# Kernel optimization log

Measured on AMD Instinct MI355X. Metric: run time of the kernel, lower is better.

The kernel has to match this reference:

```python
import jax, jax.numpy as jnp
import numpy as np

N = 50000          # residues
E = 1000000        # edges
H = 128            # hidden_channels
CUT = 11.5         # cutoff
NR = 6             # num_radial
NS = 3             # num_spherical
NPE = 16           # num_pos_emb

def swish(x):
    return x * jax.nn.sigmoid(x)

def rbf(d):
    # Bessel-style radial basis with smooth cosine cutoff, [E, NR]
    u = jnp.clip(d / CUT, 0.0, 1.0)
    n = jnp.arange(1, NR + 1, dtype=jnp.float32)
    fc = 0.5 * (jnp.cos(jnp.pi * u) + 1.0)
    return jnp.sqrt(2.0 / CUT) * jnp.sin(n * jnp.pi * u[:, None]) / (d[:, None] + 1e-6) * fc[:, None]

def angle_emb(d, ang):
    # d_angle_emb: radial x cos(l*angle) -> [E, NR*NS]
    r = rbf(d)
    l = jnp.arange(NS, dtype=jnp.float32)
    a = jnp.cos(ang[:, None] * l)
    return (r[:, :, None] * a[:, None, :]).reshape(d.shape[0], NR * NS)

def theta_phi_emb(d, theta, phi):
    # d_theta_phi_emb: radial x angular(theta) x angular(phi) -> [E, NR*NS*NS]
    r = rbf(d)
    l = jnp.arange(NS, dtype=jnp.float32)
    ct = jnp.cos(theta[:, None] * l)
    cp = jnp.cos(phi[:, None] * l)
    return jnp.einsum('en,el,em->enlm', r, ct, cp).reshape(d.shape[0], NR * NS * NS)


def setup_inputs():
    key = jax.random.key(0)
    ks = jax.random.split(key, 20)
    f32 = jnp.float32
    pos = jax.random.normal(ks[0], (N, 3), f32) * 8.0
    pos_n = pos + jax.random.normal(ks[1], (N, 3), f32) * 0.8
    pos_c = pos + jax.random.normal(ks[2], (N, 3), f32) * 0.8
    z = jax.random.randint(ks[3], (N,), 0, 26)
    bb_embs = jax.random.normal(ks[4], (N, 6), f32)
    side_chain_embs = jax.random.normal(ks[5], (N, 8), f32)
    esm_embs = jax.random.normal(ks[6], (N, 1280), f32)
    batch = jnp.zeros((N,), jnp.int32)
    edge_index = jax.random.randint(ks[7], (2, E), 0, N)
    def w(k, shape):
        return jax.random.normal(k, shape, f32) * (1.0 / np.sqrt(shape[0]))
    edge_in = NR * NS * NS + 3 * NR * NS + NPE  # 54 + 54 + 16 = 124
    params = dict(
        W_emb=w(ks[8], (26 + 6 + 8, H // 2)), b_emb=jnp.zeros((H // 2,), f32),
        W_esm=w(ks[9], (1280, H // 2)), b_esm=jnp.zeros((H // 2,), f32),
        W_edge=w(ks[10], (edge_in, H)),
        W_msg=w(ks[11], (H, H)),
        W_upd=w(ks[12], (H, H)),
        W_o0=w(ks[13], (H, H)), b_o0=jnp.zeros((H,), f32),
        W_o1=w(ks[14], (H, 32)), b_o1=jnp.zeros((32,), f32),
        W_of=w(ks[15], (32, 1)), b_of=jnp.zeros((1,), f32),
        W_n0=w(ks[16], (H, 32)), b_n0=jnp.zeros((32,), f32),
        W_nf=w(ks[17], (32, 2)), b_nf=jnp.zeros((2,), f32),
    )
    return dict(z=z, pos=pos, pos_n=pos_n, pos_c=pos_c, bb_embs=bb_embs,
                side_chain_embs=side_chain_embs, esm_embs=esm_embs,
                batch=batch, edge_index=edge_index, **params)


def reference(z, pos, pos_n, pos_c, bb_embs, side_chain_embs, esm_embs, batch,
              edge_index, W_emb, b_emb, W_esm, b_esm, W_edge, W_msg, W_upd,
              W_o0, b_o0, W_o1, b_o1, W_of, b_of, W_n0, b_n0, W_nf, b_nf):
    # --- node embedding fusion (level='allatom+esm') ---
    oh = jax.nn.one_hot(z, 26, dtype=jnp.float32)
    x_a = jnp.concatenate([oh, bb_embs, side_chain_embs], axis=1) @ W_emb + b_emb
    x_s = esm_embs @ W_esm + b_esm
    x = jnp.concatenate([x_a, x_s], axis=-1)  # [N, H]

    j, i = edge_index[0], edge_index[1]

    # --- sinusoidal positional embedding of sequence offsets ---
    dpe = (j - i).astype(jnp.float32)
    freq = jnp.exp(jnp.arange(0, NPE, 2, dtype=jnp.float32) * (-np.log(10000.0) / NPE))
    ang = dpe[:, None] * freq
    pe = jnp.concatenate([jnp.cos(ang), jnp.sin(ang)], axis=-1)  # [E, NPE]

    # --- distance / theta / phi (triplet gathers via sequence neighbors) ---
    v_ji = pos[j] - pos[i]
    dist = jnp.linalg.norm(pos[i] - pos[j], axis=1)
    refi0 = (i - 1) % N
    refi1 = (i + 1) % N
    v_r0 = pos[refi0] - pos[i]
    v_r1 = pos[refi1] - pos[i]
    a = jnp.sum(v_ji * v_r0, axis=-1)
    b = jnp.linalg.norm(jnp.cross(v_ji, v_r0), axis=-1)
    theta = jnp.arctan2(b, a)
    p1 = jnp.cross(v_r0, v_r1)
    p2 = jnp.cross(v_r0, v_ji)
    a = jnp.sum(p1 * p2, axis=-1)
    b = jnp.sum(jnp.cross(p1, p2) * v_r0, axis=-1) / (jnp.linalg.norm(v_r0, axis=-1) + 1e-7)
    phi = jnp.arctan2(b, a)
    feature0 = theta_phi_emb(dist, theta, phi)  # [E, 54]

    # --- backbone-frame Euler angles (allatom branch) ---
    o1x = pos_n[i] - pos[i]
    o1z = jnp.cross(o1x, jnp.cross(o1x, pos_c[i] - pos[i]))
    o1zl = jnp.linalg.norm(o1z, axis=1) + 1e-7
    o2x = pos_n[j] - pos[j]
    o2z = jnp.cross(o2x, jnp.cross(o2x, pos_c[j] - pos[j]))
    o2zl = jnp.linalg.norm(o2z, axis=1) + 1e-7
    nvec = jnp.cross(o1z, o2z)
    angle1 = jnp.arctan2(jnp.sum(jnp.cross(o1x, nvec) * o1z, -1) / o1zl, jnp.sum(o1x * nvec, -1))
    angle2 = jnp.arctan2(jnp.linalg.norm(nvec, axis=-1), jnp.sum(o1z * o2z, -1))
    angle3 = jnp.arctan2(jnp.sum(jnp.cross(nvec, o2x) * o2z, -1) / o2zl, jnp.sum(nvec * o2x, -1))
    feature1 = jnp.concatenate([angle_emb(dist, angle1), angle_emb(dist, angle2),
                                angle_emb(dist, angle3)], axis=1)  # [E, 54]

    # --- message passing (gather-compute-scatter stand-in for model_E) ---
    ef = swish(jnp.concatenate([feature0, feature1, pe], axis=-1) @ W_edge)  # [E, H]
    m = swish(x[j] @ W_msg) * ef
    agg = jax.ops.segment_sum(m, i, num_segments=N)
    xe = x + swish(agg @ W_upd)

    # --- output heads (dropout inactive at inference) ---
    xn = jax.nn.relu(x @ W_n0 + b_n0)
    node_out = xn @ W_nf + b_nf                   # [N, 2]
    h = jax.nn.relu(xe @ W_o0 + b_o0)
    h = jax.nn.relu(h @ W_o1 + b_o1)
    out = jax.nn.sigmoid(h @ W_of + b_of)         # [N, 1]
    return out, node_out
```

## Files before the change

### kernel.cpp

```cpp
#include <hip/hip_runtime.h>
#include <math.h>
#include <stdint.h>

#define NRES 50000
#define NEDGE 1000000
#define PI_F 3.14159265358979323846f
#define NSEG 196

typedef __attribute__((ext_vector_type(8))) short short8;
typedef __attribute__((ext_vector_type(4))) float floatx4;
typedef __attribute__((ext_vector_type(2))) short bf16x2;
typedef __attribute__((address_space(1))) bf16x2* gbf16x2p;

struct f3 { float x, y, z; };
__device__ __forceinline__ f3 ld3(const float* __restrict__ p, int i) {
  return {p[3*i+0], p[3*i+1], p[3*i+2]};
}
__device__ __forceinline__ f3 f3sub(f3 a, f3 b){ return {a.x-b.x, a.y-b.y, a.z-b.z}; }
__device__ __forceinline__ f3 f3cross(f3 a, f3 b){
  return {a.y*b.z - a.z*b.y, a.z*b.x - a.x*b.z, a.x*b.y - a.y*b.x};
}
__device__ __forceinline__ float f3dot(f3 a, f3 b){ return a.x*b.x + a.y*b.y + a.z*b.z; }
__device__ __forceinline__ float swish_fast(float v){
  return v * __builtin_amdgcn_rcpf(1.0f + __expf(-v));
}
__device__ __forceinline__ short f2bf(float f){
  unsigned u = __float_as_uint(f);
  unsigned r = (u + 0x7fffu + ((u >> 16) & 1u)) >> 16;
  return (short)r;
}
__device__ __forceinline__ float bf2f(short s){
  return __uint_as_float(((unsigned)(unsigned short)s) << 16);
}
__device__ __forceinline__ float cos_atan2(float y, float x){
  return x * __builtin_amdgcn_rsqf(fmaxf(x*x + y*y, 1e-30f));
}
__device__ __forceinline__ void atom_pk_bf16(short* addr, bf16x2 v){
  __builtin_amdgcn_global_atomic_fadd_v2bf16((gbf16x2p)(uintptr_t)addr, v);
}
__device__ __forceinline__ unsigned pkbf(float lo, float hi){
  unsigned r;
  asm("v_cvt_pk_bf16_f32 %0, %1, %2" : "=v"(r) : "v"(lo), "v"(hi));
  return r;
}

__device__ __forceinline__ void edge_features(
    int e, int j, int i,
    const float* __restrict__ pos, const float* __restrict__ posn,
    const float* __restrict__ posc, short (*sF)[136])
{
  f3 pj = ld3(pos, j), pi = ld3(pos, i);
  f3 vji = f3sub(pj, pi);
  float nji2 = f3dot(vji, vji);
  float dist = sqrtf(nji2);
  int r0i = (i == 0) ? (NRES - 1) : (i - 1);
  int r1i = (i == NRES - 1) ? 0 : (i + 1);
  f3 vr0 = f3sub(ld3(pos, r0i), pi);
  f3 vr1 = f3sub(ld3(pos, r1i), pi);
  float nr02 = f3dot(vr0, vr0);

  float ct = f3dot(vji, vr0) * __builtin_amdgcn_rsqf(fmaxf(nji2 * nr02, 1e-30f));
  f3 p1 = f3cross(vr0, vr1);
  f3 p2 = f3cross(vr0, vji);
  float pa = f3dot(p1, p2);
  float pb = f3dot(f3cross(p1, p2), vr0) / (sqrtf(nr02) + 1e-7f);
  float cp = cos_atan2(pb, pa);

  f3 pni = ld3(posn, i), pci = ld3(posc, i);
  f3 o1x = f3sub(pni, pi);
  f3 o1z = f3cross(o1x, f3cross(o1x, f3sub(pci, pi)));
  float no1z2 = f3dot(o1z, o1z);
  float o1zl = sqrtf(no1z2) + 1e-7f;
  f3 pnj = ld3(posn, j), pcj = ld3(posc, j);
  f3 o2x = f3sub(pnj, pj);
  f3 o2z = f3cross(o2x, f3cross(o2x, f3sub(pcj, pj)));
  float no2z2 = f3dot(o2z, o2z);
  float o2zl = sqrtf(no2z2) + 1e-7f;
  f3 nv = f3cross(o1z, o2z);
  float y1 = f3dot(f3cross(o1x, nv), o1z) / o1zl;
  float ca1 = cos_atan2(y1, f3dot(o1x, nv));
  float ca2 = f3dot(o1z, o2z) * __builtin_amdgcn_rsqf(fmaxf(no1z2 * no2z2, 1e-30f));
  float y3 = f3dot(f3cross(nv, o2x), o2z) / o2zl;
  float ca3 = cos_atan2(y3, f3dot(nv, o2x));

  float u = fminf(dist * (1.0f/11.5f), 1.0f);
  float spu, cpu;
  __sincosf(PI_F * u, &spu, &cpu);
  float fc = 0.5f * (cpu + 1.0f);
  float pref = 0.41702882811414954f * __builtin_amdgcn_rcpf(dist + 1e-6f) * fc;
  float rb[6];
  {
    float twoc = 2.0f * cpu;
    float s_nm1 = 0.0f, s_n = spu;
    #pragma unroll
    for (int nn = 0; nn < 6; ++nn) {
      rb[nn] = pref * s_n;
      float s_np1 = twoc * s_n - s_nm1;
      s_nm1 = s_n; s_n = s_np1;
    }
  }

  float pend = 0.0f;
  float ctv[3] = {1.0f, ct, 2.0f*ct*ct - 1.0f};
  float cpv[3] = {1.0f, cp, 2.0f*cp*cp - 1.0f};
  #pragma unroll
  for (int nn = 0; nn < 6; ++nn)
    #pragma unroll
    for (int l = 0; l < 3; ++l)
      #pragma unroll
      for (int m = 0; m < 3; ++m) {
        const int f = nn*9 + l*3 + m;
        float v = rb[nn] * ctv[l] * cpv[m];
        if (f & 1) *(unsigned*)&sF[e][f-1] = pkbf(pend, v);
        else       pend = v;
      }

  float cas[3] = {ca1, ca2, ca3};
  #pragma unroll
  for (int t = 0; t < 3; ++t) {
    float c = cas[t];
    float cav[3] = {1.0f, c, 2.0f*c*c - 1.0f};
    #pragma unroll
    for (int nn = 0; nn < 6; ++nn)
      #pragma unroll
      for (int l = 0; l < 3; ++l) {
        const int f = 54 + t*18 + nn*3 + l;
        float v = rb[nn] * cav[l];
        if (f & 1) *(unsigned*)&sF[e][f-1] = pkbf(pend, v);
        else       pend = v;
      }
  }

  const float FRQ[8] = {1.0f, 0.31622776601683794f, 0.1f, 0.03162277660168379f,
                        0.01f, 0.003162277660168379f, 0.001f, 0.0003162277660168379f};
  float dpe = (float)(j - i);
  float cb[8], sb[8];
  #pragma unroll
  for (int q = 0; q < 8; ++q) __sincosf(dpe * FRQ[q], &sb[q], &cb[q]);
  #pragma unroll
  for (int q = 0; q < 8; q += 2) {
    *(unsigned*)&sF[e][108 + q] = pkbf(cb[q], cb[q+1]);
    *(unsigned*)&sF[e][116 + q] = pkbf(sb[q], sb[q+1]);
  }
  *(unsigned*)&sF[e][124] = 0u;
  *(unsigned*)&sF[e][126] = 0u;
}

__global__ __launch_bounds__(256) void k_wprep(
    const float* __restrict__ We, const float* __restrict__ Wm,
    const float* __restrict__ Ws, const float* __restrict__ Wu,
    const float* __restrict__ Wo0, const float* __restrict__ Wn0,
    const float* __restrict__ Wo1,
    short* __restrict__ Wef, short* __restrict__ Wmf, short* __restrict__ Wsf,
    short* __restrict__ Wuf, short* __restrict__ Wo0f,
    short* __restrict__ Wn0f, short* __restrict__ Wo1f)
{
  int gid = blockIdx.x * 256 + threadIdx.x;
  const float* src; short* dst; int NT, K, N, t;
  if      (gid < 16384)  { t = gid;          src = We;  dst = Wef;  NT = 8; K = 124;  N = 128; }
  else if (gid < 32768)  { t = gid - 16384;  src = Wm;  dst = Wmf;  NT = 8; K = 128;  N = 128; }
  else if (gid < 114688) { t = gid - 32768;  src = Ws;  dst = Wsf;  NT = 4; K = 1280; N = 64;  }
  else if (gid < 131072) { t = gid - 114688; src = Wu;  dst = Wuf;  NT = 8; K = 128;  N = 128; }
  else if (gid < 147456) { t = gid - 131072; src = Wo0; dst = Wo0f; NT = 8; K = 128;  N = 128; }
  else if (gid < 151552) { t = gid - 147456; src = Wn0; dst = Wn0f; NT = 2; K = 128;  N = 32;  }
  else if (gid < 155648) { t = gid - 151552; src = Wo1; dst = Wo1f; NT = 2; K = 128;  N = 32;  }
  else return;
  int j = t & 7, lane = (t >> 3) & 63;
  int rest = t >> 9;
  int nt = rest % NT, kt = rest / NT;
  int k = kt*32 + (lane >> 4)*8 + j, n = nt*16 + (lane & 15);
  dst[t] = f2bf((k < K) ? src[k*N + n] : 0.0f);
}

__global__ __launch_bounds__(256) void k_hist(
    const int* __restrict__ ei, int* __restrict__ bins)
{
  int e = blockIdx.x * 256 + threadIdx.x;
  if (e < NEDGE) atomicAdd(&bins[ei[NEDGE + e]], 1);
}

__global__ __launch_bounds__(256) void k_scan1(
    int* __restrict__ bins, int* __restrict__ bsum)
{
  __shared__ int s[256];
  const int t = threadIdx.x, b = blockIdx.x;
  const int idx = b * 256 + t;
  int v = (idx < NRES) ? bins[idx] : 0;
  s[t] = v;
  __syncthreads();
  #pragma unroll
  for (int d = 1; d < 256; d <<= 1) {
    int add = (t >= d) ? s[t - d] : 0;
    __syncthreads();
    if (t >= d) s[t] += add;
    __syncthreads();
  }
  if (idx < NRES) bins[idx] = s[t] - v;
  if (t == 255) bsum[b] = s[255];
}

__global__ __launch_bounds__(256) void k_scan2(int* __restrict__ bsum)
{
  __shared__ int s[256];
  const int t = threadIdx.x;
  int v = (t < NSEG) ? bsum[t] : 0;
  s[t] = v;
  __syncthreads();
  #pragma unroll
  for (int d = 1; d < 256; d <<= 1) {
    int add = (t >= d) ? s[t - d] : 0;
    __syncthreads();
    if (t >= d) s[t] += add;
    __syncthreads();
  }
  if (t < NSEG) bsum[t] = s[t] - v;
}

__global__ __launch_bounds__(256) void k_scan3(
    int* __restrict__ bins, const int* __restrict__ bsum)
{
  int idx = blockIdx.x * 256 + threadIdx.x;
  if (idx < NRES) bins[idx] += bsum[blockIdx.x];
}

__global__ __launch_bounds__(256) void k_scatter(
    const int* __restrict__ ei, int* __restrict__ bins, int2* __restrict__ sij)
{
  int e = blockIdx.x * 256 + threadIdx.x;
  if (e < NEDGE) {
    int j = ei[e], i = ei[NEDGE + e];
    int slot = atomicAdd(&bins[i], 1);
    if (slot >= 0 && slot < NEDGE) sij[slot] = make_int2(j, i);
  }
}

__global__ __launch_bounds__(256) void k_xa(
    const int* __restrict__ z, const float* __restrict__ bb,
    const float* __restrict__ side, const float* __restrict__ W_emb,
    const float* __restrict__ b_emb, short* __restrict__ xb)
{
  int tid = threadIdx.x;
  int h = tid & 63;
  int n = blockIdx.x * 4 + (tid >> 6);
  if (n >= NRES) return;
  int zz = z[n];
  float acc = W_emb[zz * 64 + h] + b_emb[h];
  #pragma unroll
  for (int k = 0; k < 6; ++k) acc += bb[n*6 + k] * W_emb[(26 + k)*64 + h];
  #pragma unroll
  for (int k = 0; k < 8; ++k) acc += side[n*8 + k] * W_emb[(32 + k)*64 + h];
  xb[(size_t)n * 128 + h] = f2bf(acc);
}

__global__ __launch_bounds__(256) void k_esm(
    const float* __restrict__ esm, const short* __restrict__ Wsf,
    const float* __restrict__ b, short* __restrict__ xb)
{
  const int tid = threadIdx.x;
  const int lane = tid & 63, w = tid >> 6;
  const int quad = lane >> 4, colb = lane & 15;
  const int tile0 = blockIdx.x * 64 + w * 16;

  int arow = tile0 + colb;
  if (arow >= NRES) arow = NRES - 1;
  const float* ap = esm + (size_t)arow * 1280 + quad * 8;

  floatx4 acc[4];
  #pragma unroll
  for (int nt = 0; nt < 4; ++nt) acc[nt] = (floatx4){0.f, 0.f, 0.f, 0.f};

  for (int kt = 0; kt < 40; ++kt) {
    float4 v0 = *(const float4*)(ap + kt*32);
    float4 v1 = *(const float4*)(ap + kt*32 + 4);
    short8 a;
    a[0] = f2bf(v0.x); a[1] = f2bf(v0.y); a[2] = f2bf(v0.z); a[3] = f2bf(v0.w);
    a[4] = f2bf(v1.x); a[5] = f2bf(v1.y); a[6] = f2bf(v1.z); a[7] = f2bf(v1.w);
    #pragma unroll
    for (int nt = 0; nt < 4; ++nt) {
      short8 bf = *(const short8*)&Wsf[(size_t)((kt*4 + nt)*64 + lane)*8];
      acc[nt] = __builtin_amdgcn_mfma_f32_16x16x32_bf16(a, bf, acc[nt], 0, 0, 0);
    }
  }
  #pragma unroll
  for (int nt = 0; nt < 4; ++nt) {
    int ch = nt*16 + colb;
    float bias = b[ch];
    #pragma unroll
    for (int r = 0; r < 4; ++r) {
      int n = tile0 + quad*4 + r;
      if (n < NRES) xb[(size_t)n * 128 + 64 + ch] = f2bf(acc[nt][r] + bias);
    }
  }
}

__global__ __launch_bounds__(256) void k_node(
    const float* __restrict__ esm, const short* __restrict__ Wsf,
    const float* __restrict__ b_esm,
    const int* __restrict__ z, const float* __restrict__ bb,
    const float* __restrict__ side, const float* __restrict__ W_emb,
    const float* __restrict__ b_emb,
    const short* __restrict__ Wmf,
    short* __restrict__ xb, short* __restrict__ xmb)
{
  __shared__ __align__(16) short sX[64][136];

  const int tid = threadIdx.x;
  const int lane = tid & 63, w = tid >> 6;
  const int quad = lane >> 4, colb = lane & 15;
  const int n0 = blockIdx.x * 64;
  const int tile0 = n0 + w * 16;

  int arow = tile0 + colb;
  if (arow >= NRES) arow = NRES - 1;
  const float* ap = esm + (size_t)arow * 1280 + quad * 8;

  floatx4 acc[4];
  #pragma unroll
  for (int nt = 0; nt < 4; ++nt) acc[nt] = (floatx4){0.f, 0.f, 0.f, 0.f};

  for (int kt = 0; kt < 40; ++kt) {
    float4 v0 = *(const float4*)(ap + kt*32);
    float4 v1 = *(const float4*)(ap + kt*32 + 4);
    short8 a;
    a[0] = f2bf(v0.x); a[1] = f2bf(v0.y); a[2] = f2bf(v0.z); a[3] = f2bf(v0.w);
    a[4] = f2bf(v1.x); a[5] = f2bf(v1.y); a[6] = f2bf(v1.z); a[7] = f2bf(v1.w);
    #pragma unroll
    for (int nt = 0; nt < 4; ++nt) {
      short8 bf = *(const short8*)&Wsf[(size_t)((kt*4 + nt)*64 + lane)*8];
      acc[nt] = __builtin_amdgcn_mfma_f32_16x16x32_bf16(a, bf, acc[nt], 0, 0, 0);
    }
  }

  #pragma unroll
  for (int nt = 0; nt < 4; ++nt) {
    int ch = nt*16 + colb;
    float bias = b_esm[ch];
    #pragma unroll
    for (int r = 0; r < 4; ++r)
      sX[w*16 + quad*4 + r][64 + ch] = f2bf(acc[nt][r] + bias);
  }
  {
    int r2 = tid >> 2;
    int n2 = n0 + r2; if (n2 >= NRES) n2 = NRES - 1;
    int c0 = (tid & 3) * 16;
    int zz = z[n2];
    float bbv[6], sdv[8];
    #pragma unroll
    for (int k = 0; k < 6; ++k) bbv[k] = bb[n2*6 + k];
    #pragma unroll
    for (int k = 0; k < 8; ++k) sdv[k] = side[n2*8 + k];
    #pragma unroll
    for (int c = 0; c < 16; c += 2) {
      float v0, v1;
      #pragma unroll
      for (int h = 0; h < 2; ++h) {
        int col = c0 + c + h;
        float a2 = W_emb[zz*64 + col] + b_emb[col];
        #pragma unroll
        for (int k = 0; k < 6; ++k) a2 += bbv[k] * W_emb[(26 + k)*64 + col];
        #pragma unroll
        for (int k = 0; k < 8; ++k) a2 += sdv[k] * W_emb[(32 + k)*64 + col];
        if (h) v1 = a2; else v0 = a2;
      }
      *(unsigned*)&sX[r2][c0 + c] = pkbf(v0, v1);
    }
  }
  __syncthreads();

  #pragma unroll
  for (int it = 0; it < 4; ++it) {
    int idx = it * 256 + tid;
    int row = idx >> 4, c8 = idx & 15;
    int n = n0 + row;
    if (n < NRES) *(short8*)&xb[(size_t)n * 128 + c8*8] = *(const short8*)&sX[row][c8*8];
  }

  floatx4 accM[4][2];
  #pragma unroll
  for (int mt = 0; mt < 4; ++mt) {
    accM[mt][0] = (floatx4){0.f,0.f,0.f,0.f};
    accM[mt][1] = (floatx4){0.f,0.f,0.f,0.f};
  }
  #pragma unroll
  for (int kt = 0; kt < 4; ++kt) {
    short8 b0 = *(const short8*)&Wmf[(size_t)((kt*8 + w*2 + 0)*64 + lane)*8];
    short8 b1 = *(const short8*)&Wmf[(size_t)((kt*8 + w*2 + 1)*64 + lane)*8];
    #pragma unroll
    for (int mt = 0; mt < 4; ++mt) {
      short8 a = *(const short8*)&sX[mt*16 + colb][kt*32 + quad*8];
      accM[mt][0] = __builtin_amdgcn_mfma_f32_16x16x32_bf16(a, b0, accM[mt][0], 0, 0, 0);
      accM[mt][1] = __builtin_amdgcn_mfma_f32_16x16x32_bf16(a, b1, accM[mt][1], 0, 0, 0);
    }
  }
  __syncthreads();

  #pragma unroll
  for (int mt = 0; mt < 4; ++mt)
    #pragma unroll
    for (int nt = 0; nt < 2; ++nt)
      #pragma unroll
      for (int r = 0; r < 4; ++r)
        sX[mt*16 + quad*4 + r][w*32 + nt*16 + colb] = f2bf(swish_fast(accM[mt][nt][r]));
  __syncthreads();
  #pragma unroll
  for (int it = 0; it < 4; ++it) {
    int idx = it * 256 + tid;
    int row = idx >> 4, c8 = idx & 15;
    int n = n0 + row;
    if (n < NRES) *(short8*)&xmb[(size_t)n * 128 + c8*8] = *(const short8*)&sX[row][c8*8];
  }
}

__global__ __launch_bounds__(256, 4) void k_edge_s(
    const int2* __restrict__ sij,
    const float* __restrict__ pos,
    const float* __restrict__ posn, const float* __restrict__ posc,
    const short* __restrict__ xmb, const short* __restrict__ Wef,
    short* __restrict__ aggb)
{
  __shared__ int sJ[64];
  __shared__ int sI[64];
  __shared__ __align__(16) short sF[64][136];
  __shared__ __align__(16) short sXJ[64][136];

  const int tid = threadIdx.x;
  const int orig = blockIdx.x;
  const int xcd = orig & 7, sub = orig >> 3;
  const int wg = (xcd == 0 ? 0 : 1954 + (xcd - 1) * 1953) + sub;
  const int e0 = wg * 64;

  if (tid < 64) {
    int2 ji = sij[e0 + tid];
    int jj = ji.x, ii = ji.y;
    sJ[tid] = (jj < 0) ? 0 : ((jj >= NRES) ? NRES - 1 : jj);
    sI[tid] = (ii < 0) ? 0 : ((ii >= NRES) ? NRES - 1 : ii);
  }
  __syncthreads();

  if (tid < 64) {
    edge_features(tid, sJ[tid], sI[tid], pos, posn, posc, sF);
  } else {
    const int t2 = tid - 64;
    for (int it = 0; it < 6; ++it) {
      int idx = it * 192 + t2;
      if (idx < 1024) {
        int row = idx >> 4;
        int c8 = idx & 15;
        *(short8*)&sXJ[row][c8*8] = *(const short8*)&xmb[(size_t)sJ[row] * 128 + c8*8];
      }
    }
  }
  __syncthreads();

  const int lane = tid & 63, w = tid >> 6;
  const int quad = lane >> 4, colb = lane & 15;
  const int nb = w * 2;

  short8 bE[4][2];
  #pragma unroll
  for (int kt = 0; kt < 4; ++kt)
    #pragma unroll
    for (int nt = 0; nt < 2; ++nt)
      bE[kt][nt] = *(const short8*)&Wef[(size_t)((kt*8 + nb + nt)*64 + lane)*8];

  floatx4 accE[4][2];
  #pragma unroll
  for (int mt = 0; mt < 4; ++mt) {
    accE[mt][0] = (floatx4){0.f, 0.f, 0.f, 0.f};
    accE[mt][1] = (floatx4){0.f, 0.f, 0.f, 0.f};
  }

  #pragma unroll
  for (int kt = 0; kt < 4; ++kt) {
    #pragma unroll
    for (int mt = 0; mt < 4; ++mt) {
      short8 af = *(const short8*)&sF[mt*16 + colb][kt*32 + quad*8];
      #pragma unroll
      for (int nt = 0; nt < 2; ++nt)
        accE[mt][nt] = __builtin_amdgcn_mfma_f32_16x16x32_bf16(af, bE[kt][nt], accE[mt][nt], 0, 0, 0);
    }
  }
  __syncthreads();

  short (*sM)[136] = sF;
  #pragma unroll
  for (int mt = 0; mt < 4; ++mt)
    #pragma unroll
    for (int nt = 0; nt < 2; ++nt) {
      int ch = w*32 + nt*16 + colb;
      #pragma unroll
      for (int r = 0; r < 4; ++r) {
        int e = mt*16 + quad*4 + r;
        float mv = bf2f(sXJ[e][ch]) * swish_fast(accE[mt][nt][r]);
        sM[e][ch] = f2bf(mv);
      }
    }
  __syncthreads();

  {
    const int p = tid & 63;
    const int g = tid >> 6;
    float ax = 0.f, ay = 0.f;
    int cur = sI[g * 16];
    #pragma unroll
    for (int rr = 0; rr < 16; ++rr) {
      int row = g * 16 + rr;
      int ii = sI[row];
      if (ii != cur) {
        bf16x2 v; v[0] = f2bf(ax); v[1] = f2bf(ay);
        atom_pk_bf16(&aggb[(size_t)cur * 128 + p*2], v);
        ax = 0.f; ay = 0.f; cur = ii;
      }
      bf16x2 mv = *(const bf16x2*)&sM[row][p*2];
      ax += bf2f(mv[0]); ay += bf2f(mv[1]);
    }
    bf16x2 v; v[0] = f2bf(ax); v[1] = f2bf(ay);
    atom_pk_bf16(&aggb[(size_t)cur * 128 + p*2], v);
  }
}

__global__ __launch_bounds__(256, 4) void k_edge_b(
    const int* __restrict__ ei, const float* __restrict__ pos,
    const float* __restrict__ posn, const float* __restrict__ posc,
    const short* __restrict__ xb, const short* __restrict__ Wef,
    const short* __restrict__ Wmf, short* __restrict__ aggb)
{
  __shared__ int sJ[64];
  __shared__ int sI[64];
  __shared__ __align__(16) short sF[64][136];
  __shared__ __align__(16) short sXJ[64][136];

  const int tid = threadIdx.x;
  const int e0 = blockIdx.x * 64;

  if (tid < 64) { sJ[tid] = ei[e0 + tid]; sI[tid] = ei[NEDGE + e0 + tid]; }
  __syncthreads();

  if (tid < 64) {
    edge_features(tid, sJ[tid], sI[tid], pos, posn, posc, sF);
  } else {
    const int t2 = tid - 64;
    for (int it = 0; it < 6; ++it) {
      int idx = it * 192 + t2;
      if (idx < 1024) {
        int row = idx >> 4;
        int c8 = idx & 15;
        *(short8*)&sXJ[row][c8*8] = *(const short8*)&xb[(size_t)sJ[row] * 128 + c8*8];
      }
    }
  }
  __syncthreads();

  const int lane = tid & 63, w = tid >> 6;
  const int quad = lane >> 4, colb = lane & 15;
  const int nb = w * 2;

  short8 bE[4][2], bM[4][2];
  #pragma unroll
  for (int kt = 0; kt < 4; ++kt)
    #pragma unroll
    for (int nt = 0; nt < 2; ++nt) {
      bE[kt][nt] = *(const short8*)&Wef[(size_t)((kt*8 + nb + nt)*64 + lane)*8];
      bM[kt][nt] = *(const short8*)&Wmf[(size_t)((kt*8 + nb + nt)*64 + lane)*8];
    }

  floatx4 accE[4][2], accM[4][2];
  #pragma unroll
  for (int mt = 0; mt < 4; ++mt)
    #pragma unroll
    for (int nt = 0; nt < 2; ++nt) {
      accE[mt][nt] = (floatx4){0.f, 0.f, 0.f, 0.f};
      accM[mt][nt] = (floatx4){0.f, 0.f, 0.f, 0.f};
    }

  #pragma unroll
  for (int kt = 0; kt < 4; ++kt) {
    #pragma unroll
    for (int mt = 0; mt < 4; ++mt) {
      short8 af = *(const short8*)&sF [mt*16 + colb][kt*32 + quad*8];
      short8 ax = *(const short8*)&sXJ[mt*16 + colb][kt*32 + quad*8];
      #pragma unroll
      for (int nt = 0; nt < 2; ++nt) {
        accE[mt][nt] = __builtin_amdgcn_mfma_f32_16x16x32_bf16(af, bE[kt][nt], accE[mt][nt], 0, 0, 0);
        accM[mt][nt] = __builtin_amdgcn_mfma_f32_16x16x32_bf16(ax, bM[kt][nt], accM[mt][nt], 0, 0, 0);
      }
    }
  }
  __syncthreads();

  short (*sM)[136] = sXJ;
  #pragma unroll
  for (int mt = 0; mt < 4; ++mt)
    #pragma unroll
    for (int nt = 0; nt < 2; ++nt) {
      int ch = w*32 + nt*16 + colb;
      #pragma unroll
      for (int r = 0; r < 4; ++r) {
        int e = mt*16 + quad*4 + r;
        sM[e][ch] = f2bf(swish_fast(accM[mt][nt][r]) * swish_fast(accE[mt][nt][r]));
      }
    }
  __syncthreads();

  #pragma unroll
  for (int it = 0; it < 16; ++it) {
    int flat = it * 256 + tid;
    int row = flat >> 6, p = flat & 63;
    bf16x2 v = *(const bf16x2*)&sM[row][p*2];
    atom_pk_bf16(&aggb[(size_t)sI[row] * 128 + p*2], v);
  }
}

__global__ __launch_bounds__(256) void k_upd(
    const short* __restrict__ xb, const short* __restrict__ aggb,
    const short* __restrict__ Wuf, const short* __restrict__ Wo0f,
    const short* __restrict__ Wn0f, const short* __restrict__ Wo1f,
    const float* __restrict__ bn0, const float* __restrict__ Wnf,
    const float* __restrict__ bnf, const float* __restrict__ bo0,
    const float* __restrict__ bo1, const float* __restrict__ Wof,
    const float* __restrict__ bof, float* __restrict__ out0,
    float* __restrict__ out1)
{
  __shared__ __align__(16) short sA[64][136];
  __shared__ __align__(16) short sX[64][136];
  __shared__ float sS[64][33];

  const int tid = threadIdx.x;
  const int lane = tid & 63, w = tid >> 6;
  const int quad = lane >> 4, colb = lane & 15;
  const int n0 = blockIdx.x * 64;

  #pragma unroll
  for (int it = 0; it < 4; ++it) {
    int idx = it * 256 + tid;
    int row = idx >> 4, c8 = idx & 15;
    int n = n0 + row;
    short8 va = (short8)(short)0, vx = (short8)(short)0;
    if (n < NRES) {
      va = *(const short8*)&aggb[(size_t)n * 128 + c8*8];
      vx = *(const short8*)&xb  [(size_t)n * 128 + c8*8];
    }
    *(short8*)&sA[row][c8*8] = va;
    *(short8*)&sX[row][c8*8] = vx;
  }
  __syncthreads();

  {
    floatx4 accN[2];
    accN[0] = (floatx4){0.f,0.f,0.f,0.f}; accN[1] = (floatx4){0.f,0.f,0.f,0.f};
    #pragma unroll
    for (int kt = 0; kt < 4; ++kt) {
      short8 a = *(const short8*)&sX[w*16 + colb][kt*32 + quad*8];
      #pragma unroll
      for (int nt = 0; nt < 2; ++nt) {
        short8 bf = *(const short8*)&Wn0f[(size_t)((kt*2 + nt)*64 + lane)*8];
        accN[nt] = __builtin_amdgcn_mfma_f32_16x16x32_bf16(a, bf, accN[nt], 0, 0, 0);
      }
    }
    #pragma unroll
    for (int nt = 0; nt < 2; ++nt) {
      int col = nt*16 + colb;
      float bias = bn0[col];
      #pragma unroll
      for (int r = 0; r < 4; ++r)
        sS[w*16 + quad*4 + r][col] = fmaxf(accN[nt][r] + bias, 0.0f);
    }
  }
  __syncthreads();
  if (tid < 128) {
    int row = tid >> 1, oc = tid & 1;
    int n = n0 + row;
    if (n < NRES) {
      float a2 = bnf[oc];
      #pragma unroll
      for (int k = 0; k < 32; ++k) a2 += sS[row][k] * Wnf[k*2 + oc];
      out1[(size_t)n * 2 + oc] = a2;
    }
  }

  floatx4 acc1[4][2];
  #pragma unroll
  for (int mt = 0; mt < 4; ++mt) {
    acc1[mt][0] = (floatx4){0.f,0.f,0.f,0.f};
    acc1[mt][1] = (floatx4){0.f,0.f,0.f,0.f};
  }
  #pragma unroll
  for (int kt = 0; kt < 4; ++kt) {
    short8 b0 = *(const short8*)&Wuf[(size_t)((kt*8 + w*2 + 0)*64 + lane)*8];
    short8 b1 = *(const short8*)&Wuf[(size_t)((kt*8 + w*2 + 1)*64 + lane)*8];
    #pragma unroll
    for (int mt = 0; mt < 4; ++mt) {
      short8 a = *(const short8*)&sA[mt*16 + colb][kt*32 + quad*8];
      acc1[mt][0] = __builtin_amdgcn_mfma_f32_16x16x32_bf16(a, b0, acc1[mt][0], 0, 0, 0);
      acc1[mt][1] = __builtin_amdgcn_mfma_f32_16x16x32_bf16(a, b1, acc1[mt][1], 0, 0, 0);
    }
  }
  __syncthreads();
  #pragma unroll
  for (int mt = 0; mt < 4; ++mt)
    #pragma unroll
    for (int nt = 0; nt < 2; ++nt)
      #pragma unroll
      for (int r = 0; r < 4; ++r) {
        int row = mt*16 + quad*4 + r, col = w*32 + nt*16 + colb;
        float xv = bf2f(sX[row][col]);
        sA[row][col] = f2bf(xv + swish_fast(acc1[mt][nt][r]));
      }
  __syncthreads();

  floatx4 acc2[4][2];
  #pragma unroll
  for (int mt = 0; mt < 4; ++mt) {
    acc2[mt][0] = (floatx4){0.f,0.f,0.f,0.f};
    acc2[mt][1] = (floatx4){0.f,0.f,0.f,0.f};
  }
  #pragma unroll
  for (int kt = 0; kt < 4; ++kt) {
    short8 b0 = *(const short8*)&Wo0f[(size_t)((kt*8 + w*2 + 0)*64 + lane)*8];
    short8 b1 = *(const short8*)&Wo0f[(size_t)((kt*8 + w*2 + 1)*64 + lane)*8];
    #pragma unroll
    for (int mt = 0; mt < 4; ++mt) {
      short8 a = *(const short8*)&sA[mt*16 + colb][kt*32 + quad*8];
      acc2[mt][0] = __builtin_amdgcn_mfma_f32_16x16x32_bf16(a, b0, acc2[mt][0], 0, 0, 0);
      acc2[mt][1] = __builtin_amdgcn_mfma_f32_16x16x32_bf16(a, b1, acc2[mt][1], 0, 0, 0);
    }
  }
  __syncthreads();
  #pragma unroll
  for (int mt = 0; mt < 4; ++mt)
    #pragma unroll
    for (int nt = 0; nt < 2; ++nt) {
      int col = w*32 + nt*16 + colb;
      float bias = bo0[col];
      #pragma unroll
      for (int r = 0; r < 4; ++r) {
        int row = mt*16 + quad*4 + r;
        sX[row][col] = f2bf(fmaxf(acc2[mt][nt][r] + bias, 0.0f));
      }
    }
  __syncthreads();

  {
    floatx4 accH[2];
    accH[0] = (floatx4){0.f,0.f,0.f,0.f}; accH[1] = (floatx4){0.f,0.f,0.f,0.f};
    #pragma unroll
    for (int kt = 0; kt < 4; ++kt) {
      short8 a = *(const short8*)&sX[w*16 + colb][kt*32 + quad*8];
      #pragma unroll
      for (int nt = 0; nt < 2; ++nt) {
        short8 bf = *(const short8*)&Wo1f[(size_t)((kt*2 + nt)*64 + lane)*8];
        accH[nt] = __builtin_amdgcn_mfma_f32_16x16x32_bf16(a, bf, accH[nt], 0, 0, 0);
      }
    }
    __syncthreads();
    #pragma unroll
    for (int nt = 0; nt < 2; ++nt) {
      int col = nt*16 + colb;
      float bias = bo1[col];
      #pragma unroll
      for (int r = 0; r < 4; ++r)
        sS[w*16 + quad*4 + r][col] = fmaxf(accH[nt][r] + bias, 0.0f);
    }
  }
  __syncthreads();

  if (tid < 64) {
    int n = n0 + tid;
    if (n < NRES) {
      float a2 = bof[0];
      #pragma unroll
      for (int k = 0; k < 32; ++k) a2 += sS[tid][k] * Wof[k];
      out0[n] = 1.0f / (1.0f + expf(-a2));
    }
  }
}

extern "C" void kernel_launch(void* const* d_in, const int* in_sizes, int n_in,
                              void* d_out, int out_size, void* d_ws, size_t ws_size,
                              hipStream_t stream) {
  (void)in_sizes; (void)n_in; (void)out_size;
  const int*   z     = (const int*)  d_in[0];
  const float* pos   = (const float*)d_in[1];
  const float* posn  = (const float*)d_in[2];
  const float* posc  = (const float*)d_in[3];
  const float* bb    = (const float*)d_in[4];
  const float* side  = (const float*)d_in[5];
  const float* esm   = (const float*)d_in[6];
  const int*   ei    = (const int*)  d_in[8];
  const float* W_emb = (const float*)d_in[9];
  const float* b_emb = (const float*)d_in[10];
  const float* W_esm = (const float*)d_in[11];
  const float* b_esm = (const float*)d_in[12];
  const float* W_edge= (const float*)d_in[13];
  const float* W_msg = (const float*)d_in[14];
  const float* W_upd = (const float*)d_in[15];
  const float* W_o0  = (const float*)d_in[16];
  const float* b_o0  = (const float*)d_in[17];
  const float* W_o1  = (const float*)d_in[18];
  const float* b_o1  = (const float*)d_in[19];
  const float* W_of  = (const float*)d_in[20];
  const float* b_of  = (const float*)d_in[21];
  const float* W_n0  = (const float*)d_in[22];
  const float* b_n0  = (const float*)d_in[23];
  const float* W_nf  = (const float*)d_in[24];
  const float* b_nf  = (const float*)d_in[25];

  float* out0 = (float*)d_out;
  float* out1 = out0 + NRES;
  char* ws = (char*)d_ws;

  const bool full = (ws_size >= (size_t)46912096);

  if (full) {
    short* xb   = (short*)ws;
    short* aggb = (short*)(ws + 12800000);
    short* xmb  = (short*)(ws + 25600000);
    short* Wef  = (short*)(ws + 38400000);
    short* Wmf  = (short*)(ws + 38432768);
    short* Wsf  = (short*)(ws + 38465536);
    short* Wuf  = (short*)(ws + 38629376);
    short* Wo0f = (short*)(ws + 38662144);
    short* Wn0f = (short*)(ws + 38694912);
    short* Wo1f = (short*)(ws + 38703104);
    int*   bins = (int*)  (ws + 38711296);
    int*   bsum = (int*)  (ws + 38911296);
    int2*  sij  = (int2*) (ws + 38912096);

    hipMemsetAsync(aggb, 0, (size_t)NRES * 128 * sizeof(short), stream);
    hipMemsetAsync(bins, 0, (size_t)NRES * sizeof(int), stream);

    k_wprep  <<<608, 256, 0, stream>>>(W_edge, W_msg, W_esm, W_upd, W_o0, W_n0, W_o1,
                                       Wef, Wmf, Wsf, Wuf, Wo0f, Wn0f, Wo1f);
    k_hist   <<<3907, 256, 0, stream>>>(ei, bins);
    k_scan1  <<<NSEG, 256, 0, stream>>>(bins, bsum);
    k_scan2  <<<1,    256, 0, stream>>>(bsum);
    k_scan3  <<<NSEG, 256, 0, stream>>>(bins, bsum);
    k_scatter<<<3907, 256, 0, stream>>>(ei, bins, sij);
    k_node   <<<782,  256, 0, stream>>>(esm, Wsf, b_esm, z, bb, side, W_emb, b_emb,
                                        Wmf, xb, xmb);
    k_edge_s <<<15625, 256, 0, stream>>>(sij, pos, posn, posc, xmb, Wef, aggb);
    k_upd    <<<782,   256, 0, stream>>>(xb, aggb, Wuf, Wo0f, Wn0f, Wo1f,
                                         b_n0, W_nf, b_nf, b_o0, b_o1, W_of, b_of,
                                         out0, out1);
  } else {
    short* xb   = (short*)ws;
    short* aggb = (short*)(ws + 12800000);
    short* Wef  = (short*)(ws + 25600000);
    short* Wmf  = (short*)(ws + 25632768);
    short* Wsf  = (short*)(ws + 25665536);
    short* Wuf  = (short*)(ws + 25829376);
    short* Wo0f = (short*)(ws + 25862144);
    short* Wn0f = (short*)(ws + 25894912);
    short* Wo1f = (short*)(ws + 25903104);

    hipMemsetAsync(aggb, 0, (size_t)NRES * 128 * sizeof(short), stream);

    k_wprep <<<608, 256, 0, stream>>>(W_edge, W_msg, W_esm, W_upd, W_o0, W_n0, W_o1,
                                      Wef, Wmf, Wsf, Wuf, Wo0f, Wn0f, Wo1f);
    k_xa    <<<12500, 256, 0, stream>>>(z, bb, side, W_emb, b_emb, xb);
    k_esm   <<<782,   256, 0, stream>>>(esm, Wsf, b_esm, xb);
    k_edge_b<<<15625, 256, 0, stream>>>(ei, pos, posn, posc, xb, Wef, Wmf, aggb);
    k_upd   <<<782,   256, 0, stream>>>(xb, aggb, Wuf, Wo0f, Wn0f, Wo1f,
                                        b_n0, W_nf, b_nf, b_o0, b_o1, W_of, b_of,
                                        out0, out1);
  }
}
```

Measured before the change: 706.6 us.

## Split k_node ESM GEMM reduction across two wave groups with 512 threads

k_node now runs 512 threads per block, so each 16-row tile is computed by two waves that each take half of the 1280-wide ESM reduction. The two partial sums are combined through a new shared-memory buffer. The loop also prefetches the next float4 pair of ESM inputs in registers, and the embedding and W_msg work is spread over 8 waves. The aim is more memory-level parallelism and shorter per-wave serial chains in this bandwidth-bound node kernel, at the cost of extra shared memory and a synchronization.

Measured after the change: 706.7 us. Within noise of the previous version (+0.0%).

```diff
diff --git a/kernel.cpp b/kernel.cpp
--- a/kernel.cpp
+++ b/kernel.cpp
@@ -293,7 +293,7 @@
   }
 }
 
-__global__ __launch_bounds__(256) void k_node(
+__global__ __launch_bounds__(512) void k_node(
     const float* __restrict__ esm, const short* __restrict__ Wsf,
     const float* __restrict__ b_esm,
     const int* __restrict__ z, const float* __restrict__ bb,
@@ -303,46 +303,67 @@
     short* __restrict__ xb, short* __restrict__ xmb)
 {
   __shared__ __align__(16) short sX[64][136];
+  __shared__ float sP[4][16][68];
 
   const int tid = threadIdx.x;
   const int lane = tid & 63, w = tid >> 6;
   const int quad = lane >> 4, colb = lane & 15;
+  const int t = w & 3, kh = w >> 2;
   const int n0 = blockIdx.x * 64;
-  const int tile0 = n0 + w * 16;
+  const int tile0 = n0 + t * 16;
 
   int arow = tile0 + colb;
   if (arow >= NRES) arow = NRES - 1;
-  const float* ap = esm + (size_t)arow * 1280 + quad * 8;
+  const float* ap = esm + (size_t)arow * 1280 + kh * 640 + quad * 8;
 
   floatx4 acc[4];
   #pragma unroll
   for (int nt = 0; nt < 4; ++nt) acc[nt] = (floatx4){0.f, 0.f, 0.f, 0.f};
 
-  for (int kt = 0; kt < 40; ++kt) {
-    float4 v0 = *(const float4*)(ap + kt*32);
-    float4 v1 = *(const float4*)(ap + kt*32 + 4);
+  float4 v0 = *(const float4*)(ap);
+  float4 v1 = *(const float4*)(ap + 4);
+  for (int kt = 0; kt < 20; ++kt) {
+    float4 nv0 = v0, nv1 = v1;
+    if (kt < 19) {
+      nv0 = *(const float4*)(ap + (kt+1)*32);
+      nv1 = *(const float4*)(ap + (kt+1)*32 + 4);
+    }
     short8 a;
     a[0] = f2bf(v0.x); a[1] = f2bf(v0.y); a[2] = f2bf(v0.z); a[3] = f2bf(v0.w);
     a[4] = f2bf(v1.x); a[5] = f2bf(v1.y); a[6] = f2bf(v1.z); a[7] = f2bf(v1.w);
+    const int kc = kh*20 + kt;
     #pragma unroll
     for (int nt = 0; nt < 4; ++nt) {
-      short8 bf = *(const short8*)&Wsf[(size_t)((kt*4 + nt)*64 + lane)*8];
+      short8 bf = *(const short8*)&Wsf[(size_t)((kc*4 + nt)*64 + lane)*8];
       acc[nt] = __builtin_amdgcn_mfma_f32_16x16x32_bf16(a, bf, acc[nt], 0, 0, 0);
     }
-  }
-
-  #pragma unroll
-  for (int nt = 0; nt < 4; ++nt) {
-    int ch = nt*16 + colb;
-    float bias = b_esm[ch];
-    #pragma unroll
-    for (int r = 0; r < 4; ++r)
-      sX[w*16 + quad*4 + r][64 + ch] = f2bf(acc[nt][r] + bias);
+    v0 = nv0; v1 = nv1;
+  }
+
+  if (kh == 1) {
+    #pragma unroll
+    for (int nt = 0; nt < 4; ++nt)
+      #pragma unroll
+      for (int r = 0; r < 4; ++r)
+        sP[t][quad*4 + r][nt*16 + colb] = acc[nt][r];
+  }
+  __syncthreads();
+
+  if (kh == 0) {
+    #pragma unroll
+    for (int nt = 0; nt < 4; ++nt) {
+      int ch = nt*16 + colb;
+      float bias = b_esm[ch];
+      #pragma unroll
+      for (int r = 0; r < 4; ++r)
+        sX[t*16 + quad*4 + r][64 + ch] =
+            f2bf(acc[nt][r] + sP[t][quad*4 + r][ch] + bias);
+    }
   }
   {
-    int r2 = tid >> 2;
+    int r2 = tid >> 3;
     int n2 = n0 + r2; if (n2 >= NRES) n2 = NRES - 1;
-    int c0 = (tid & 3) * 16;
+    int c0 = (tid & 7) * 8;
     int zz = z[n2];
     float bbv[6], sdv[8];
     #pragma unroll
@@ -350,8 +371,8 @@
     #pragma unroll
     for (int k = 0; k < 8; ++k) sdv[k] = side[n2*8 + k];
     #pragma unroll
-    for (int c = 0; c < 16; c += 2) {
-      float v0, v1;
+    for (int c = 0; c < 8; c += 2) {
+      float u0, u1;
       #pragma unroll
       for (int h = 0; h < 2; ++h) {
         int col = c0 + c + h;
@@ -360,36 +381,31 @@
         for (int k = 0; k < 6; ++k) a2 += bbv[k] * W_emb[(26 + k)*64 + col];
         #pragma unroll
         for (int k = 0; k < 8; ++k) a2 += sdv[k] * W_emb[(32 + k)*64 + col];
-        if (h) v1 = a2; else v0 = a2;
-      }
-      *(unsigned*)&sX[r2][c0 + c] = pkbf(v0, v1);
-    }
-  }
-  __syncthreads();
-
-  #pragma unroll
-  for (int it = 0; it < 4; ++it) {
-    int idx = it * 256 + tid;
+        if (h) u1 = a2; else u0 = a2;
+      }
+      *(unsigned*)&sX[r2][c0 + c] = pkbf(u0, u1);
+    }
+  }
+  __syncthreads();
+
+  #pragma unroll
+  for (int it = 0; it < 2; ++it) {
+    int idx = it * 512 + tid;
     int row = idx >> 4, c8 = idx & 15;
     int n = n0 + row;
     if (n < NRES) *(short8*)&xb[(size_t)n * 128 + c8*8] = *(const short8*)&sX[row][c8*8];
   }
 
-  floatx4 accM[4][2];
-  #pragma unroll
-  for (int mt = 0; mt < 4; ++mt) {
-    accM[mt][0] = (floatx4){0.f,0.f,0.f,0.f};
-    accM[mt][1] = (floatx4){0.f,0.f,0.f,0.f};
-  }
+  floatx4 accM[4];
+  #pragma unroll
+  for (int mt = 0; mt < 4; ++mt) accM[mt] = (floatx4){0.f,0.f,0.f,0.f};
   #pragma unroll
   for (int kt = 0; kt < 4; ++kt) {
-    short8 b0 = *(const short8*)&Wmf[(size_t)((kt*8 + w*2 + 0)*64 + lane)*8];
-    short8 b1 = *(const short8*)&Wmf[(size_t)((kt*8 + w*2 + 1)*64 + lane)*8];
+    short8 b0 = *(const short8*)&Wmf[(size_t)((kt*8 + w)*64 + lane)*8];
     #pragma unroll
     for (int mt = 0; mt < 4; ++mt) {
       short8 a = *(const short8*)&sX[mt*16 + colb][kt*32 + quad*8];
-      accM[mt][0] = __builtin_amdgcn_mfma_f32_16x16x32_bf16(a, b0, accM[mt][0], 0, 0, 0);
-      accM[mt][1] = __builtin_amdgcn_mfma_f32_16x16x32_bf16(a, b1, accM[mt][1], 0, 0, 0);
+      accM[mt] = __builtin_amdgcn_mfma_f32_16x16x32_bf16(a, b0, accM[mt], 0, 0, 0);
     }
   }
   __syncthreads();
@@ -397,14 +413,12 @@
   #pragma unroll
   for (int mt = 0; mt < 4; ++mt)
     #pragma unroll
-    for (int nt = 0; nt < 2; ++nt)
-      #pragma unroll
-      for (int r = 0; r < 4; ++r)
-        sX[mt*16 + quad*4 + r][w*32 + nt*16 + colb] = f2bf(swish_fast(accM[mt][nt][r]));
-  __syncthreads();
-  #pragma unroll
-  for (int it = 0; it < 4; ++it) {
-    int idx = it * 256 + tid;
+    for (int r = 0; r < 4; ++r)
+      sX[mt*16 + quad*4 + r][w*16 + colb] = f2bf(swish_fast(accM[mt][r]));
+  __syncthreads();
+  #pragma unroll
+  for (int it = 0; it < 2; ++it) {
+    int idx = it * 512 + tid;
     int row = idx >> 4, c8 = idx & 15;
     int n = n0 + row;
     if (n < NRES) *(short8*)&xmb[(size_t)n * 128 + c8*8] = *(const short8*)&sX[row][c8*8];
@@ -836,7 +850,7 @@
     k_scan2  <<<1,    256, 0, stream>>>(bsum);
     k_scan3  <<<NSEG, 256, 0, stream>>>(bins, bsum);
     k_scatter<<<3907, 256, 0, stream>>>(ei, bins, sij);
-    k_node   <<<782,  256, 0, stream>>>(esm, Wsf, b_esm, z, bb, side, W_emb, b_emb,
+    k_node   <<<782,  512, 0, stream>>>(esm, Wsf, b_esm, z, bb, side, W_emb, b_emb,
                                         Wmf, xb, xmb);
     k_edge_s <<<15625, 256, 0, stream>>>(sij, pos, posn, posc, xmb, Wef, aggb);
     k_upd    <<<782,   256, 0, stream>>>(xb, aggb, Wuf, Wo0f, Wn0f, Wo1f,
```
